# Kernel optimization log

Hardware: AMD Instinct MI355X
Metric: run time of the kernel (lower is better)

The kernel has to match this reference:

```python
import jax, jax.numpy as jnp
import numpy as np

N = 8192      # num nodes
D = 128       # feature dim (input_dim)
E = 262144    # num edges (avg degree 32)
P = 4         # num perspectives (num_pers)
EPSILON = 0.3 # similarity threshold (args.epsilon)


def setup_inputs() -> dict:
    key = jax.random.key(0)
    k1, k2, k3, k4 = jax.random.split(key, 4)
    x = jax.random.normal(k1, (N, D), dtype=jnp.float32)
    ori_index = jax.random.randint(k2, (2, E), 0, N, dtype=jnp.int32)
    ori_weight = jax.random.uniform(k3, (E,), dtype=jnp.float32)
    w_pers = jax.random.normal(k4, (P, D), dtype=jnp.float32)  # weighted-cosine perspective weights
    return {"x": x, "ori_index": ori_index, "ori_weight": ori_weight, "w_pers": w_pers}


def reference(x, ori_index, ori_weight, w_pers):
    n = x.shape[0]
    # to_dense_adj: scatter edge weights into dense [N, N] adjacency (duplicate edges add)
    ori_g = jnp.zeros((n, n), dtype=x.dtype).at[ori_index[0], ori_index[1]].add(ori_weight)

    # GraphLearner (weighted multi-perspective cosine):
    # reweight features per perspective, L2-normalize, cosine sim, mean over perspectives
    xw = x[None, :, :] * w_pers[:, None, :]                              # [P, N, D]
    xn = xw / jnp.maximum(jnp.linalg.norm(xw, axis=-1, keepdims=True), 1e-12)
    sim = jnp.mean(jnp.einsum('pnd,pmd->pnm', xn, xn), axis=0)           # [N, N]
    # epsilon-thresholded learned graph
    sim_g = jnp.where(sim > EPSILON, sim, jnp.zeros_like(sim))

    # purified(sim, ori_g, epsilon): keep original edges where sim*ori_g > epsilon
    pur_g = jnp.where(sim * ori_g > EPSILON, ori_g, jnp.zeros_like(sim))
    new_g = pur_g + sim_g
    # dense_to_sparse has data-dependent output size; return the dense refined
    # adjacency (same information: edges = nonzero(new_g), weights = values).
    return new_g
```

## Files before the change

kernel.cpp:

```cpp
#include <hip/hip_runtime.h>
#include <hip/hip_bf16.h>
#include <stdint.h>

#define N_NODES 8192
#define DIM     128
#define KTOT    512
#define NEDGE   262144
#define EPS     0.3f
#define FIX_DELTA 0.008f
#define FIX_CAP (1u << 19)
#define XCAP    (1u << 18)
#define LCAP    512
#define HASH_BITS 19
#define HASH_SLOTS (1u << HASH_BITS)

typedef unsigned int u32;
typedef unsigned short u16;
typedef __attribute__((ext_vector_type(8))) short short8;
typedef __attribute__((ext_vector_type(4))) float float4v;

#define OFF_YF  0u
#define OFF_YB  16777216u
#define OFF_CTR 25165824u
#define OFF_HK  25166080u
#define OFF_HV  27263232u
#define OFF_FL  29360384u
#define OFF_UL  31457536u
#define OFF_XL  32506112u
#define MEMSET_OFF OFF_CTR
#define MEMSET_BYTES (OFF_FL - OFF_CTR)

__device__ __forceinline__ u16 f2bf(float f) {
    u32 b = __builtin_bit_cast(u32, f);
    b += 0x7fffu + ((b >> 16) & 1u);
    return (u16)(b >> 16);
}

__global__ void prep_y(const float* __restrict__ x, const float* __restrict__ wp,
                       float* __restrict__ yf, u16* __restrict__ yb) {
    int node = blockIdx.x * 4 + (threadIdx.x >> 6);
    int lane = threadIdx.x & 63;
    float x0 = x[node * DIM + lane];
    float x1 = x[node * DIM + lane + 64];
    for (int p = 0; p < 4; ++p) {
        float v0 = x0 * wp[p * DIM + lane];
        float v1 = x1 * wp[p * DIM + lane + 64];
        float ss = v0 * v0 + v1 * v1;
        #pragma unroll
        for (int o = 1; o < 64; o <<= 1) ss += __shfl_xor(ss, o, 64);
        float scale = 0.5f / fmaxf(sqrtf(ss), 1e-12f);
        float y0 = v0 * scale, y1 = v1 * scale;
        int base = node * KTOT + p * DIM;
        yf[base + lane] = y0;       yf[base + lane + 64] = y1;
        yb[base + lane] = f2bf(y0); yb[base + lane + 64] = f2bf(y1);
    }
}

__global__ void edge_insert(const int* __restrict__ idx, const float* __restrict__ w,
                            u32* __restrict__ hkey, float* __restrict__ hval,
                            u32* __restrict__ ucnt, u32* __restrict__ ulist) {
    int e = blockIdx.x * 256 + threadIdx.x;
    u32 cell = (u32)(idx[e] * N_NODES + idx[NEDGE + e]);
    float wv = w[e];
    u32 key = cell + 1u;
    u32 h = (cell * 2654435761u) >> (32 - HASH_BITS);
    while (true) {
        u32 old = atomicCAS(&hkey[h], 0u, key);
        if (old == 0u) { ulist[atomicAdd(ucnt, 1u)] = h; atomicAdd(&hval[h], wv); break; }
        if (old == key) { atomicAdd(&hval[h], wv); break; }
        h = (h + 1u) & (HASH_SLOTS - 1u);
    }
}

#define TM  128
#define BK  64

__global__ __launch_bounds__(256)
void gemm_sim(const u16* __restrict__ yb, float* __restrict__ out,
              u32* __restrict__ fcnt, u32* __restrict__ flst) {
    __shared__ __align__(16) u16 As[TM * BK];
    __shared__ __align__(16) u16 Bs[TM * BK];
    __shared__ u32 s_cnt, s_base;
    __shared__ u32 s_list[LCAP];
    int bm = blockIdx.y, bn = blockIdx.x;
    int tid = threadIdx.x;
    int lane = tid & 63, wid = tid >> 6;
    int wm = wid >> 1, wn = wid & 1;
    if (tid == 0) s_cnt = 0;

    float4v acc[4][4] = {};
    const u16* arow = yb + (size_t)(bm * TM) * KTOT;
    const u16* brow = yb + (size_t)(bn * TM) * KTOT;

    for (int kt = 0; kt < KTOT / BK; ++kt) {
        __syncthreads();
        #pragma unroll
        for (int q = 0; q < 4; ++q) {
            int c = q * 256 + wid * 64 + lane;
            int row = c >> 3;
            int kg = (c & 7) ^ (row & 7);
            __builtin_amdgcn_global_load_lds(
                (const __attribute__((address_space(1))) void*)(const void*)(arow + (size_t)row * KTOT + kt * BK + kg * 8),
                (__attribute__((address_space(3))) void*)(void*)(As + (q * 256 + wid * 64) * 8),
                16, 0, 0);
            __builtin_amdgcn_global_load_lds(
                (const __attribute__((address_space(1))) void*)(const void*)(brow + (size_t)row * KTOT + kt * BK + kg * 8),
                (__attribute__((address_space(3))) void*)(void*)(Bs + (q * 256 + wid * 64) * 8),
                16, 0, 0);
        }
        __syncthreads();
        #pragma unroll
        for (int kk = 0; kk < 2; ++kk) {
            short8 af[4], bfr[4];
            int kg2 = kk * 4 + (lane >> 4);
            int mrow = wm * 64 + (lane & 15);
            int ncol = wn * 64 + (lane & 15);
            #pragma unroll
            for (int i = 0; i < 4; ++i) {
                int ra = mrow + i * 16, rb = ncol + i * 16;
                af[i]  = *(const short8*)&As[ra * BK + ((kg2 ^ (ra & 7)) * 8)];
                bfr[i] = *(const short8*)&Bs[rb * BK + ((kg2 ^ (rb & 7)) * 8)];
            }
            #pragma unroll
            for (int i = 0; i < 4; ++i)
                #pragma unroll
                for (int j = 0; j < 4; ++j)
                    acc[i][j] = __builtin_amdgcn_mfma_f32_16x16x32_bf16(
                        af[i], bfr[j], acc[i][j], 0, 0, 0);
        }
    }

    int quad = lane >> 4, lcol = lane & 15;
    #pragma unroll
    for (int i = 0; i < 4; ++i)
        #pragma unroll
        for (int j = 0; j < 4; ++j) {
            int gr0 = bm * TM + wm * 64 + i * 16 + quad * 4;
            int gc  = bn * TM + wn * 64 + j * 16 + lcol;
            #pragma unroll
            for (int r = 0; r < 4; ++r) {
                float s = acc[i][j][r];
                out[(size_t)(gr0 + r) * N_NODES + gc] = s > EPS ? s : 0.f;
                if (fabsf(s - EPS) < FIX_DELTA) {
                    u32 li = atomicAdd(&s_cnt, 1u);
                    u32 cell = (u32)((gr0 + r) * N_NODES + gc);
                    if (li < LCAP) s_list[li] = cell;
                    else { u32 g = atomicAdd(fcnt, 1u); if (g < FIX_CAP) flst[g] = cell; }
                }
            }
        }
    __syncthreads();
    u32 cnt = s_cnt < LCAP ? s_cnt : LCAP;
    if (tid == 0) s_base = atomicAdd(fcnt, cnt);
    __syncthreads();
    for (u32 t = tid; t < cnt; t += 256) {
        u32 g = s_base + t;
        if (g < FIX_CAP) flst[g] = s_list[t];
    }
}

__device__ __forceinline__ float dot_exact(const float* __restrict__ yf,
                                           u32 i, u32 j, int tl) {
    const float4v* ri = (const float4v*)(yf + (size_t)i * KTOT);
    const float4v* rj = (const float4v*)(yf + (size_t)j * KTOT);
    float4v p = {};
    #pragma unroll
    for (int q = 0; q < 8; ++q) p += ri[q * 16 + tl] * rj[q * 16 + tl];
    float s = p.x + p.y + p.z + p.w;
    #pragma unroll
    for (int o = 8; o >= 1; o >>= 1) s += __shfl_xor(s, o, 16);
    return s;
}

__global__ void fixup(const float* __restrict__ yf, const u32* __restrict__ fcnt,
                      const u32* __restrict__ flst, float* __restrict__ out) {
    u32 count = *fcnt; if (count > FIX_CAP) count = FIX_CAP;
    int team = (blockIdx.x * 256 + threadIdx.x) >> 4;
    int tl = threadIdx.x & 15;
    int nteams = gridDim.x * 16;
    for (u32 t = team; t < count; t += nteams) {
        u32 cell = flst[t];
        u32 i = cell >> 13, j = cell & 8191u;
        float s = dot_exact(yf, i, j, tl);
        if (tl == 0) out[cell] = s > EPS ? s : 0.f;
    }
}

__global__ void edge_fast(const u32* __restrict__ hkey, const float* __restrict__ hval,
                          const u32* __restrict__ ucnt, const u32* __restrict__ ulist,
                          float* __restrict__ out,
                          u32* __restrict__ xcnt, u32* __restrict__ xlist) {
    u32 count = *ucnt;
    for (u32 t = blockIdx.x * 256 + threadIdx.x; t < count; t += gridDim.x * 256) {
        u32 h = ulist[t];
        u32 cell = hkey[h] - 1u;
        float a = hval[h];
        float sg = out[cell];
        bool hard = (a > 1.0f) ||
                    (sg > 0.f && fabsf(sg * a - EPS) < FIX_DELTA * a + 1e-6f) ||
                    (sg == 0.f && a > 0.97f);
        if (hard) {
            u32 g = atomicAdd(xcnt, 1u);
            if (g < XCAP) xlist[g] = h;
        } else if (sg > 0.f) {
            out[cell] = sg + ((sg * a > EPS) ? a : 0.f);
        }
    }
}

__global__ void edge_exact(const float* __restrict__ yf, const u32* __restrict__ hkey,
                           const float* __restrict__ hval, const u32* __restrict__ xcnt,
                           const u32* __restrict__ xlist, float* __restrict__ out) {
    u32 count = *xcnt; if (count > XCAP) count = XCAP;
    int team = (blockIdx.x * 256 + threadIdx.x) >> 4;
    int tl = threadIdx.x & 15;
    int nteams = gridDim.x * 16;
    for (u32 t = team; t < count; t += nteams) {
        u32 h = xlist[t];
        u32 cell = hkey[h] - 1u;
        float a = hval[h];
        u32 i = cell >> 13, j = cell & 8191u;
        float s = dot_exact(yf, i, j, tl);
        if (tl == 0) {
            float v = s > EPS ? s : 0.f;
            if (s * a > EPS) v += a;
            out[cell] = v;
        }
    }
}

extern "C" void kernel_launch(void* const* d_in, const int* in_sizes, int n_in,
                              void* d_out, int out_size, void* d_ws, size_t ws_size,
                              hipStream_t stream) {
    const float* x  = (const float*)d_in[0];
    const int*   oi = (const int*)d_in[1];
    const float* ow = (const float*)d_in[2];
    const float* wp = (const float*)d_in[3];
    float* out = (float*)d_out;
    char* ws = (char*)d_ws;
    float* yf = (float*)(ws + OFF_YF);
    u16*   yb = (u16*)(ws + OFF_YB);
    u32*   fc = (u32*)(ws + OFF_CTR);
    u32*   uc = (u32*)(ws + OFF_CTR + 4);
    u32*   xc = (u32*)(ws + OFF_CTR + 8);
    u32*   hk = (u32*)(ws + OFF_HK);
    float* hv = (float*)(ws + OFF_HV);
    u32*   fl = (u32*)(ws + OFF_FL);
    u32*   ul = (u32*)(ws + OFF_UL);
    u32*   xl = (u32*)(ws + OFF_XL);

    prep_y<<<N_NODES / 4, 256, 0, stream>>>(x, wp, yf, yb);
    hipMemsetAsync(ws + MEMSET_OFF, 0, MEMSET_BYTES, stream);
    edge_insert<<<NEDGE / 256, 256, 0, stream>>>(oi, ow, hk, hv, uc, ul);
    gemm_sim<<<dim3(N_NODES / TM, N_NODES / TM), 256, 0, stream>>>(yb, out, fc, fl);
    fixup<<<2048, 256, 0, stream>>>(yf, fc, fl, out);
    edge_fast<<<1024, 256, 0, stream>>>(hk, hv, uc, ul, out, xc, xl);
    edge_exact<<<256, 256, 0, stream>>>(yf, hk, hv, xc, xl, out);
}
```

Baseline: 526.2 us.

## Fuse fixup with edge pass, drop LDS in GEMM, narrow fixup band

Zeroing of the counters and hash table moves into extra blocks of prep_y, replacing the separate memset. The fixup and edge_fast kernels are merged into one launch, split by block index. Because fixup may now rewrite out[cell] while the edge pass reads it, cells whose similarity sits near the threshold are routed to the exact edge path. The GEMM stops staging tiles in shared memory and loads bf16 fragments straight from global memory into double-buffered registers. FIX_DELTA is also narrowed so fewer cells need exact recomputation, which assumes the bf16 error stays inside the smaller band and risks wrong outputs if it does not.

```diff
diff --git a/kernel.cpp b/kernel.cpp
--- a/kernel.cpp
+++ b/kernel.cpp
@@ -7,7 +7,7 @@
 #define KTOT    512
 #define NEDGE   262144
 #define EPS     0.3f
-#define FIX_DELTA 0.008f
+#define FIX_DELTA 0.0043f
 #define FIX_CAP (1u << 19)
 #define XCAP    (1u << 18)
 #define LCAP    512
@@ -27,8 +27,7 @@
 #define OFF_FL  29360384u
 #define OFF_UL  31457536u
 #define OFF_XL  32506112u
-#define MEMSET_OFF OFF_CTR
-#define MEMSET_BYTES (OFF_FL - OFF_CTR)
+#define ZERO_VEC4 262160u
 
 __device__ __forceinline__ u16 f2bf(float f) {
     u32 b = __builtin_bit_cast(u32, f);
@@ -37,7 +36,14 @@
 }
 
 __global__ void prep_y(const float* __restrict__ x, const float* __restrict__ wp,
-                       float* __restrict__ yf, u16* __restrict__ yb) {
+                       float* __restrict__ yf, u16* __restrict__ yb,
+                       uint4* __restrict__ zbase) {
+    if (blockIdx.x >= 2048) {
+        for (u32 idx = (blockIdx.x - 2048) * 256 + threadIdx.x; idx < ZERO_VEC4;
+             idx += 512 * 256)
+            zbase[idx] = make_uint4(0, 0, 0, 0);
+        return;
+    }
     int node = blockIdx.x * 4 + (threadIdx.x >> 6);
     int lane = threadIdx.x & 63;
     float x0 = x[node * DIM + lane];
@@ -72,14 +78,12 @@
     }
 }
 
-#define TM  128
-#define BK  64
+#define BM 128
+#define BN 128
 
 __global__ __launch_bounds__(256)
 void gemm_sim(const u16* __restrict__ yb, float* __restrict__ out,
               u32* __restrict__ fcnt, u32* __restrict__ flst) {
-    __shared__ __align__(16) u16 As[TM * BK];
-    __shared__ __align__(16) u16 Bs[TM * BK];
     __shared__ u32 s_cnt, s_base;
     __shared__ u32 s_list[LCAP];
     int bm = blockIdx.y, bn = blockIdx.x;
@@ -87,63 +91,51 @@
     int lane = tid & 63, wid = tid >> 6;
     int wm = wid >> 1, wn = wid & 1;
     if (tid == 0) s_cnt = 0;
+    int rquad = lane >> 4, r16 = lane & 15;
+
+    const u16* abase = yb + (size_t)(bm * BM + wm * 64 + r16) * KTOT + rquad * 8;
+    const u16* bbase = yb + (size_t)(bn * BN + wn * 64 + r16) * KTOT + rquad * 8;
 
     float4v acc[4][4] = {};
-    const u16* arow = yb + (size_t)(bm * TM) * KTOT;
-    const u16* brow = yb + (size_t)(bn * TM) * KTOT;
-
-    for (int kt = 0; kt < KTOT / BK; ++kt) {
-        __syncthreads();
-        #pragma unroll
-        for (int q = 0; q < 4; ++q) {
-            int c = q * 256 + wid * 64 + lane;
-            int row = c >> 3;
-            int kg = (c & 7) ^ (row & 7);
-            __builtin_amdgcn_global_load_lds(
-                (const __attribute__((address_space(1))) void*)(const void*)(arow + (size_t)row * KTOT + kt * BK + kg * 8),
-                (__attribute__((address_space(3))) void*)(void*)(As + (q * 256 + wid * 64) * 8),
-                16, 0, 0);
-            __builtin_amdgcn_global_load_lds(
-                (const __attribute__((address_space(1))) void*)(const void*)(brow + (size_t)row * KTOT + kt * BK + kg * 8),
-                (__attribute__((address_space(3))) void*)(void*)(Bs + (q * 256 + wid * 64) * 8),
-                16, 0, 0);
-        }
-        __syncthreads();
-        #pragma unroll
-        for (int kk = 0; kk < 2; ++kk) {
-            short8 af[4], bfr[4];
-            int kg2 = kk * 4 + (lane >> 4);
-            int mrow = wm * 64 + (lane & 15);
-            int ncol = wn * 64 + (lane & 15);
+    short8 af[2][4], bfr[2][4];
+    #pragma unroll
+    for (int i = 0; i < 4; ++i) {
+        af[0][i]  = *(const short8*)(abase + (size_t)i * 16 * KTOT);
+        bfr[0][i] = *(const short8*)(bbase + (size_t)i * 16 * KTOT);
+    }
+    #pragma unroll
+    for (int kk = 0; kk < 16; ++kk) {
+        int cur = kk & 1, nxt = cur ^ 1;
+        if (kk < 15) {
+            int ko = (kk + 1) * 32;
             #pragma unroll
             for (int i = 0; i < 4; ++i) {
-                int ra = mrow + i * 16, rb = ncol + i * 16;
-                af[i]  = *(const short8*)&As[ra * BK + ((kg2 ^ (ra & 7)) * 8)];
-                bfr[i] = *(const short8*)&Bs[rb * BK + ((kg2 ^ (rb & 7)) * 8)];
+                af[nxt][i]  = *(const short8*)(abase + ko + (size_t)i * 16 * KTOT);
+                bfr[nxt][i] = *(const short8*)(bbase + ko + (size_t)i * 16 * KTOT);
             }
+        }
+        #pragma unroll
+        for (int i = 0; i < 4; ++i)
             #pragma unroll
-            for (int i = 0; i < 4; ++i)
-                #pragma unroll
-                for (int j = 0; j < 4; ++j)
-                    acc[i][j] = __builtin_amdgcn_mfma_f32_16x16x32_bf16(
-                        af[i], bfr[j], acc[i][j], 0, 0, 0);
-        }
-    }
-
-    int quad = lane >> 4, lcol = lane & 15;
+            for (int j = 0; j < 4; ++j)
+                acc[i][j] = __builtin_amdgcn_mfma_f32_16x16x32_bf16(
+                    af[cur][i], bfr[cur][j], acc[i][j], 0, 0, 0);
+    }
+
+    int quad = rquad, lcol = r16;
     #pragma unroll
     for (int i = 0; i < 4; ++i)
         #pragma unroll
         for (int j = 0; j < 4; ++j) {
-            int gr0 = bm * TM + wm * 64 + i * 16 + quad * 4;
-            int gc  = bn * TM + wn * 64 + j * 16 + lcol;
+            int gr0 = bm * BM + wm * 64 + i * 16 + quad * 4;
+            int gc  = bn * BN + wn * 64 + j * 16 + lcol;
             #pragma unroll
             for (int r = 0; r < 4; ++r) {
                 float s = acc[i][j][r];
                 out[(size_t)(gr0 + r) * N_NODES + gc] = s > EPS ? s : 0.f;
                 if (fabsf(s - EPS) < FIX_DELTA) {
+                    u32 cell = (u32)((gr0 + r) * N_NODES + gc);
                     u32 li = atomicAdd(&s_cnt, 1u);
-                    u32 cell = (u32)((gr0 + r) * N_NODES + gc);
                     if (li < LCAP) s_list[li] = cell;
                     else { u32 g = atomicAdd(fcnt, 1u); if (g < FIX_CAP) flst[g] = cell; }
                 }
@@ -172,38 +164,40 @@
     return s;
 }
 
-__global__ void fixup(const float* __restrict__ yf, const u32* __restrict__ fcnt,
-                      const u32* __restrict__ flst, float* __restrict__ out) {
-    u32 count = *fcnt; if (count > FIX_CAP) count = FIX_CAP;
-    int team = (blockIdx.x * 256 + threadIdx.x) >> 4;
-    int tl = threadIdx.x & 15;
-    int nteams = gridDim.x * 16;
-    for (u32 t = team; t < count; t += nteams) {
-        u32 cell = flst[t];
-        u32 i = cell >> 13, j = cell & 8191u;
-        float s = dot_exact(yf, i, j, tl);
-        if (tl == 0) out[cell] = s > EPS ? s : 0.f;
-    }
-}
-
-__global__ void edge_fast(const u32* __restrict__ hkey, const float* __restrict__ hval,
-                          const u32* __restrict__ ucnt, const u32* __restrict__ ulist,
-                          float* __restrict__ out,
-                          u32* __restrict__ xcnt, u32* __restrict__ xlist) {
-    u32 count = *ucnt;
-    for (u32 t = blockIdx.x * 256 + threadIdx.x; t < count; t += gridDim.x * 256) {
-        u32 h = ulist[t];
-        u32 cell = hkey[h] - 1u;
-        float a = hval[h];
-        float sg = out[cell];
-        bool hard = (a > 1.0f) ||
-                    (sg > 0.f && fabsf(sg * a - EPS) < FIX_DELTA * a + 1e-6f) ||
-                    (sg == 0.f && a > 0.97f);
-        if (hard) {
-            u32 g = atomicAdd(xcnt, 1u);
-            if (g < XCAP) xlist[g] = h;
-        } else if (sg > 0.f) {
-            out[cell] = sg + ((sg * a > EPS) ? a : 0.f);
+__global__ void fix_and_edges(const float* __restrict__ yf,
+                              const u32* __restrict__ fcnt, const u32* __restrict__ flst,
+                              const u32* __restrict__ hkey, const float* __restrict__ hval,
+                              const u32* __restrict__ ucnt, const u32* __restrict__ ulist,
+                              float* __restrict__ out,
+                              u32* __restrict__ xcnt, u32* __restrict__ xlist) {
+    if (blockIdx.x < 1024) {
+        u32 count = *fcnt; if (count > FIX_CAP) count = FIX_CAP;
+        int team = (blockIdx.x * 256 + threadIdx.x) >> 4;
+        int tl = threadIdx.x & 15;
+        int nteams = 1024 * 16;
+        for (u32 t = team; t < count; t += nteams) {
+            u32 cell = flst[t];
+            u32 i = cell >> 13, j = cell & 8191u;
+            float s = dot_exact(yf, i, j, tl);
+            if (tl == 0) out[cell] = s > EPS ? s : 0.f;
+        }
+    } else {
+        u32 count = *ucnt;
+        for (u32 t = (blockIdx.x - 1024) * 256 + threadIdx.x; t < count; t += 512 * 256) {
+            u32 h = ulist[t];
+            u32 cell = hkey[h] - 1u;
+            float a = hval[h];
+            float sg = out[cell];
+            bool hard = (a > 1.0f) ||
+                        (fabsf(sg - EPS) < FIX_DELTA + 1e-6f) ||
+                        (sg > 0.f && fabsf(sg * a - EPS) < FIX_DELTA * a + 1e-6f) ||
+                        (sg == 0.f && a > 0.97f);
+            if (hard) {
+                u32 g = atomicAdd(xcnt, 1u);
+                if (g < XCAP) xlist[g] = h;
+            } else if (sg > 0.f) {
+                out[cell] = sg + ((sg * a > EPS) ? a : 0.f);
+            }
         }
     }
 }
@@ -249,11 +243,9 @@
     u32*   ul = (u32*)(ws + OFF_UL);
     u32*   xl = (u32*)(ws + OFF_XL);
 
-    prep_y<<<N_NODES / 4, 256, 0, stream>>>(x, wp, yf, yb);
-    hipMemsetAsync(ws + MEMSET_OFF, 0, MEMSET_BYTES, stream);
+    prep_y<<<2560, 256, 0, stream>>>(x, wp, yf, yb, (uint4*)(ws + OFF_CTR));
     edge_insert<<<NEDGE / 256, 256, 0, stream>>>(oi, ow, hk, hv, uc, ul);
-    gemm_sim<<<dim3(N_NODES / TM, N_NODES / TM), 256, 0, stream>>>(yb, out, fc, fl);
-    fixup<<<2048, 256, 0, stream>>>(yf, fc, fl, out);
-    edge_fast<<<1024, 256, 0, stream>>>(hk, hv, uc, ul, out, xc, xl);
+    gemm_sim<<<dim3(N_NODES / BN, N_NODES / BM), 256, 0, stream>>>(yb, out, fc, fl);
+    fix_and_edges<<<1536, 256, 0, stream>>>(yf, fc, fl, hk, hv, uc, ul, out, xc, xl);
     edge_exact<<<256, 256, 0, stream>>>(yf, hk, hv, xc, xl, out);
 }
```

Result: slower. 642.6 us (+22.1%).
